# Performance work log

Measured on AMD Instinct MI355X. Metric: run time of the kernel, lower is better.

Reference implementation:

```python
import jax, jax.numpy as jnp
import numpy as np
from jax import lax

B, T, H, THETA_DIM = 64, 2048, 256, 5
L1, L2, OUT = 256, 256, 1


def _p(key, shape, fan_in):
    return jax.random.normal(key, shape, dtype=jnp.float32) / np.sqrt(fan_in)


def setup_inputs() -> dict:
    key = jax.random.key(0)
    ks = jax.random.split(key, 16)
    inp = {
        "x": jax.random.normal(ks[0], (B, T), dtype=jnp.float32),
        "theta": jax.random.normal(ks[1], (B, THETA_DIM), dtype=jnp.float32),
        # LSTM layer 0 (input dim 1): gate order [i, f, g, o]
        "Wx0": _p(ks[2], (1, 4 * H), 1),
        "Wh0": _p(ks[3], (H, 4 * H), H),
        "b0": jnp.zeros((4 * H,), dtype=jnp.float32),
        # LSTM layer 1 (input dim H)
        "Wx1": _p(ks[4], (H, 4 * H), H),
        "Wh1": _p(ks[5], (H, 4 * H), H),
        "b1": jnp.zeros((4 * H,), dtype=jnp.float32),
        # theta projector Dense(H)
        "Wtp": _p(ks[6], (THETA_DIM, H), THETA_DIM),
        "btp": jnp.zeros((H,), dtype=jnp.float32),
        # MLP head: concat(H + H) -> 256 -> 256 -> 1
        "Wl1": _p(ks[7], (2 * H, L1), 2 * H),
        "bl1": jnp.zeros((L1,), dtype=jnp.float32),
        "Wl2": _p(ks[8], (L1, L2), L1),
        "bl2": jnp.zeros((L2,), dtype=jnp.float32),
        "Wo": _p(ks[9], (L2, OUT), L2),
        "bo": jnp.zeros((OUT,), dtype=jnp.float32),
    }
    return inp


def _lstm_layer(x_seq, Wx, Wh, b):
    # x_seq: [B, T, D]. Precompute input-to-gate GEMM once (big, batched),
    # leaving only the small recurrent matmul inside the scan.
    xg = jnp.einsum('btd,dg->btg', x_seq, Wx) + b  # [B, T, 4H]
    bsz = x_seq.shape[0]
    h = Wh.shape[0]
    c0 = jnp.zeros((bsz, h), dtype=x_seq.dtype)
    h0 = jnp.zeros((bsz, h), dtype=x_seq.dtype)

    def step(carry, xg_t):
        c, hh = carry
        gates = xg_t + hh @ Wh  # [B, 4H]
        i, f, g, o = jnp.split(gates, 4, axis=-1)
        c = jax.nn.sigmoid(f) * c + jax.nn.sigmoid(i) * jnp.tanh(g)
        hh = jax.nn.sigmoid(o) * jnp.tanh(c)
        return (c, hh), hh

    _, hs = lax.scan(step, (c0, h0), jnp.swapaxes(xg, 0, 1))  # hs: [T, B, H]
    return jnp.swapaxes(hs, 0, 1)  # [B, T, H]


def reference(x, theta, Wx0, Wh0, b0, Wx1, Wh1, b1, Wtp, btp,
              Wl1, bl1, Wl2, bl2, Wo, bo):
    h = x[:, :, None]  # [B, T, 1] (module expands 2-D input)
    h = _lstm_layer(h, Wx0, Wh0, b0)
    h = _lstm_layer(h, Wx1, Wh1, b1)
    h = jnp.mean(h, axis=1)  # mean_aggregation=True -> [B, H]
    tproj = theta @ Wtp + btp  # [B, H]
    z = jnp.concatenate([h, tproj], axis=-1)  # [B, 2H]
    z = jax.nn.elu(z @ Wl1 + bl1)
    z = jax.nn.elu(z @ Wl2 + bl2)
    return z @ Wo + bo  # [B, 1]
```

## Files before the change

### kernel.cpp

```cpp
#include <hip/hip_runtime.h>
#include <hip/hip_bf16.h>


#define BB 64
#define TT 2048
#define HH 256
#define D0 16
#define D1 4

typedef short s16x8 __attribute__((ext_vector_type(8)));
typedef float f32x4 __attribute__((ext_vector_type(4)));

__device__ inline unsigned short f2bf(float f) {
  unsigned u = __float_as_uint(f);
  u += 0x7fff + ((u >> 16) & 1);
  return (unsigned short)(u >> 16);
}
__device__ inline float sigm(float x) { return 1.f / (1.f + __expf(-x)); }
__device__ inline float tanh_f(float x) { return 1.f - 2.f / (__expf(2.f * x) + 1.f); }

__device__ inline unsigned long long ld64(const unsigned int* p) {
  return __hip_atomic_load((const unsigned long long*)p, __ATOMIC_RELAXED,
                           __HIP_MEMORY_SCOPE_AGENT);
}
__device__ inline void st32(unsigned int* p, unsigned int v) {
  __hip_atomic_store(p, v, __ATOMIC_RELAXED, __HIP_MEMORY_SCOPE_AGENT);
}
__device__ inline void st32i(int* p, int v) {
  __hip_atomic_store(p, v, __ATOMIC_RELAXED, __HIP_MEMORY_SCOPE_AGENT);
}
__device__ inline int ld32i(const int* p) {
  return __hip_atomic_load(p, __ATOMIC_RELAXED, __HIP_MEMORY_SCOPE_AGENT);
}
__device__ inline void wg_bar() {
  asm volatile("s_waitcnt lgkmcnt(0)" ::: "memory");
  __builtin_amdgcn_sched_barrier(0);
  __builtin_amdgcn_s_barrier();
  __builtin_amdgcn_sched_barrier(0);
}
__device__ inline bool tag2ok(unsigned long long q, unsigned int tg) {
  return (((q >> 16) & 0xFFFFu) == tg) & ((unsigned)(q >> 48) == tg);
}

#define MFMA(a, b, c) __builtin_amdgcn_mfma_f32_16x16x32_bf16((a), (b), (c), 0, 0, 0)

__global__ void xt_kernel(const float* __restrict__ x, float* __restrict__ xT) {
  int i = blockIdx.x * 256 + threadIdx.x;
  int b = i & 63, t = i >> 6;
  xT[(size_t)t * BB + b] = x[(size_t)b * TT + t];
}

__global__ __launch_bounds__(512, 1)
void lstm_kernel(const float* __restrict__ Wx0, const float* __restrict__ Wh0,
                 const float* __restrict__ b0v,
                 const float* __restrict__ Wx1, const float* __restrict__ Wh1,
                 const float* __restrict__ b1v,
                 const float* __restrict__ xT,
                 unsigned int* __restrict__ seqring,
                 unsigned int* __restrict__ h1ring,
                 float* __restrict__ hmean, int* prog)
{
  __shared__ __align__(16) char Ab [8192];
  __shared__ __align__(16) char Ab1[8192];
  __shared__ float gbuf[16][4][66];

  const int tid  = threadIdx.x;
  const int lane = tid & 63;
  const int w    = tid >> 6;
  const int u16  = lane & 15;
  const int kgrp = lane >> 4;
  const int arow = lane & 15;
  const int bid  = blockIdx.x;

  if (bid < 8) {
    const int g = bid >> 1, ho = bid & 1, po = 1 - ho;
    const int U = ho * 128 + w * 16 + u16;
    s16x8 bw[32];
#pragma unroll
    for (int n = 0; n < 4; ++n)
#pragma unroll
      for (int ph = 0; ph < 2; ++ph)
#pragma unroll
        for (int i = 0; i < 4; ++i) {
          const int ks = (ph == 0 ? ho : po) * 4 + i;
          const int col = n * 256 + U;
#pragma unroll
          for (int j = 0; j < 8; ++j)
            bw[n * 8 + ph * 4 + i][j] =
                (short)f2bf(Wh0[(size_t)(ks * 32 + kgrp * 8 + j) * 1024 + col]);
        }
    float bE[4], xE[4];
#pragma unroll
    for (int n = 0; n < 4; ++n) { bE[n] = b0v[n * 256 + U]; xE[n] = Wx0[n * 256 + U]; }

    unsigned int* sr = seqring + (size_t)g * D0 * 4096;
    const int srow = tid >> 5, spc = (tid & 31) * 4;
    float cL[4] = {0.f, 0.f, 0.f, 0.f};
    unsigned long long pq0 = 0, pq1 = 0;

    for (int t = 0; t < TT; ++t) {
      if ((t & 7) == 0 && t >= 16 && tid < 4)
        while (ld32i(&prog[(g * 4 + tid) * 16]) < t - 8) __builtin_amdgcn_s_sleep(8);
      wg_bar();

      const unsigned int* sb = sr + ((t - 1) & (D0 - 1)) * 4096 + srow * 256 + po * 128 + spc;
      unsigned long long r0 = 0, r1 = 0;
      if (t > 0) { r0 = ld64(sb); r1 = ld64(sb + 2); }
      float xr[4];
#pragma unroll
      for (int r = 0; r < 4; ++r) xr[r] = xT[(size_t)t * BB + g * 16 + kgrp * 4 + r];

      f32x4 acc[4] = {{0,0,0,0},{0,0,0,0},{0,0,0,0},{0,0,0,0}};
      if (t > 0) {
        s16x8 ao[4];
#pragma unroll
        for (int i = 0; i < 4; ++i) {
          const int ks = ho * 4 + i;
          ao[i] = *(const s16x8*)(Ab + ((arow * 512 + (ks * 32 + kgrp * 8) * 2) ^ ((arow & 7) << 4)));
        }
#pragma unroll
        for (int i = 0; i < 4; ++i)
#pragma unroll
          for (int n = 0; n < 4; ++n) acc[n] = MFMA(ao[i], bw[n * 8 + i], acc[n]);
        const unsigned int tg = (unsigned int)t;
        unsigned long long q0 = pq0, q1 = pq1;
        for (;;) {
          if (__all(tag2ok(q0, tg) & tag2ok(q1, tg))) break;
          q0 = r0; q1 = r1;
          r0 = ld64(sb); r1 = ld64(sb + 2);
        }
        const unsigned int lo = (unsigned)(q0 & 0xFFFF) | (((unsigned)(q0 >> 32) & 0xFFFF) << 16);
        const unsigned int hi = (unsigned)(q1 & 0xFFFF) | (((unsigned)(q1 >> 32) & 0xFFFF) << 16);
        *(uint2*)(Ab + ((srow * 512 + (po * 128 + spc) * 2) ^ ((srow & 7) << 4))) = (uint2){lo, hi};
      }
      wg_bar();
      if (t > 0) {
        s16x8 ap[4];
#pragma unroll
        for (int i = 0; i < 4; ++i) {
          const int ks = po * 4 + i;
          ap[i] = *(const s16x8*)(Ab + ((arow * 512 + (ks * 32 + kgrp * 8) * 2) ^ ((arow & 7) << 4)));
        }
#pragma unroll
        for (int i = 0; i < 4; ++i)
#pragma unroll
          for (int n = 0; n < 4; ++n) acc[n] = MFMA(ap[i], bw[n * 8 + 4 + i], acc[n]);
      }
      const unsigned int tagw = (unsigned)(t + 1) << 16;
#pragma unroll
      for (int r = 0; r < 4; ++r) {
        const int row = kgrp * 4 + r;
        const float gi = acc[0][r] + bE[0] + xr[r] * xE[0];
        const float gf = acc[1][r] + bE[1] + xr[r] * xE[1];
        const float gg = acc[2][r] + bE[2] + xr[r] * xE[2];
        const float go = acc[3][r] + bE[3] + xr[r] * xE[3];
        cL[r] = sigm(gf) * cL[r] + sigm(gi) * tanh_f(gg);
        const float hv = sigm(go) * tanh_f(cL[r]);
        const unsigned short hb = f2bf(hv);
        st32(sr + (t & (D0 - 1)) * 4096 + row * 256 + U, tagw | hb);
        *(unsigned short*)(Ab + ((row * 512 + U * 2) ^ ((row & 7) << 4))) = hb;
      }
      {
        const unsigned int* pb = sr + (t & (D0 - 1)) * 4096 + srow * 256 + po * 128 + spc;
        pq0 = ld64(pb); pq1 = ld64(pb + 2);
      }
    }
  } else {
    const int idx = bid - 8, g = idx >> 2, q = idx & 3;
    const int gp = w >> 2;
    const int uo = (w & 3) * 16;
    const int ub = q * 64;
    s16x8 bw[2][16];
#pragma unroll
    for (int nt = 0; nt < 2; ++nt)
#pragma unroll
      for (int ks = 0; ks < 16; ++ks) {
        const int col = (2 * gp + nt) * 256 + ub + uo + u16;
#pragma unroll
        for (int j = 0; j < 8; ++j) {
          const int k = (ks & 7) * 32 + kgrp * 8 + j;
          bw[nt][ks][j] = (short)f2bf((ks < 8) ? Wx1[(size_t)k * 1024 + col]
                                               : Wh1[(size_t)k * 1024 + col]);
        }
      }
    const int eur = tid >> 5, eu2 = (tid & 31) * 2;
    float bE[4][2];
#pragma unroll
    for (int ga = 0; ga < 4; ++ga)
#pragma unroll
      for (int uu = 0; uu < 2; ++uu)
        bE[ga][uu] = b1v[ga * 256 + ub + eu2 + uu];

    unsigned int* sr = seqring + (size_t)g * D0 * 4096;
    unsigned int* hr = h1ring  + (size_t)g * D1 * 4096;
    const int srow = tid >> 5, sc8 = (tid & 31) * 8;
    float cL[2] = {0.f, 0.f}, hs[2] = {0.f, 0.f};
    unsigned long long qh0[4], qh1[4];

    {
      const unsigned int* sb = sr + srow * 256 + sc8;
#pragma unroll
      for (int i = 0; i < 4; ++i) qh0[i] = ld64(sb + i * 2);
    }

    for (int t = 0; t < TT; ++t) {
      if ((t & 3) == 3 && tid == 0) st32i(&prog[(g * 4 + q) * 16], t);
      const unsigned int* sbh1 = hr + ((t - 1) & (D1 - 1)) * 4096 + srow * 256 + sc8;
      unsigned long long rh1[4];
      if (t > 0) {
#pragma unroll
        for (int i = 0; i < 4; ++i) rh1[i] = ld64(sbh1 + i * 2);
      }
      {
        const unsigned int* sb = sr + (t & (D0 - 1)) * 4096 + srow * 256 + sc8;
        const unsigned int tg = (unsigned int)(t + 1);
        for (;;) {
          bool ok = true;
#pragma unroll
          for (int i = 0; i < 4; ++i) ok &= tag2ok(qh0[i], tg);
          if (__all(ok)) break;
#pragma unroll
          for (int i = 0; i < 4; ++i) qh0[i] = ld64(sb + i * 2);
        }
        unsigned int wv[4];
#pragma unroll
        for (int i = 0; i < 4; ++i)
          wv[i] = (unsigned)(qh0[i] & 0xFFFF) | (((unsigned)(qh0[i] >> 32) & 0xFFFF) << 16);
        *(uint4*)(Ab + ((srow * 512 + sc8 * 2) ^ ((srow & 7) << 4))) =
            (uint4){wv[0], wv[1], wv[2], wv[3]};
      }
      wg_bar();
      f32x4 acc0 = {0,0,0,0}, acc1 = {0,0,0,0};
      {
        s16x8 a[8];
#pragma unroll
        for (int ks = 0; ks < 8; ++ks)
          a[ks] = *(const s16x8*)(Ab + ((arow * 512 + (ks * 32 + kgrp * 8) * 2) ^ ((arow & 7) << 4)));
#pragma unroll
        for (int ks = 0; ks < 8; ++ks) {
          acc0 = MFMA(a[ks], bw[0][ks], acc0);
          acc1 = MFMA(a[ks], bw[1][ks], acc1);
        }
      }
      if (t > 0) {
        const unsigned int tg = (unsigned int)t;
        for (;;) {
          bool ok = true;
#pragma unroll
          for (int i = 0; i < 4; ++i) ok &= tag2ok(qh1[i], tg);
          if (__all(ok)) break;
#pragma unroll
          for (int i = 0; i < 4; ++i) qh1[i] = rh1[i];
#pragma unroll
          for (int i = 0; i < 4; ++i) rh1[i] = ld64(sbh1 + i * 2);
        }
        unsigned int wv[4];
#pragma unroll
        for (int i = 0; i < 4; ++i)
          wv[i] = (unsigned)(qh1[i] & 0xFFFF) | (((unsigned)(qh1[i] >> 32) & 0xFFFF) << 16);
        *(uint4*)(Ab1 + ((srow * 512 + sc8 * 2) ^ ((srow & 7) << 4))) =
            (uint4){wv[0], wv[1], wv[2], wv[3]};
      }
      wg_bar();
      if (t > 0) {
        s16x8 a[8];
#pragma unroll
        for (int kk = 0; kk < 8; ++kk)
          a[kk] = *(const s16x8*)(Ab1 + ((arow * 512 + (kk * 32 + kgrp * 8) * 2) ^ ((arow & 7) << 4)));
#pragma unroll
        for (int kk = 0; kk < 8; ++kk) {
          acc0 = MFMA(a[kk], bw[0][8 + kk], acc0);
          acc1 = MFMA(a[kk], bw[1][8 + kk], acc1);
        }
      }
#pragma unroll
      for (int r = 0; r < 4; ++r) {
        gbuf[kgrp * 4 + r][2 * gp + 0][uo + u16] = acc0[r];
        gbuf[kgrp * 4 + r][2 * gp + 1][uo + u16] = acc1[r];
      }
      wg_bar();

      unsigned short hb[2];
#pragma unroll
      for (int uu = 0; uu < 2; ++uu) {
        const int u = eu2 + uu;
        const float gi = gbuf[eur][0][u] + bE[0][uu];
        const float gf = gbuf[eur][1][u] + bE[1][uu];
        const float gg = gbuf[eur][2][u] + bE[2][uu];
        const float go = gbuf[eur][3][u] + bE[3][uu];
        cL[uu] = sigm(gf) * cL[uu] + sigm(gi) * tanh_f(gg);
        const float hv = sigm(go) * tanh_f(cL[uu]);
        hs[uu] += hv;
        hb[uu] = f2bf(hv);
      }
      const unsigned int tagw = (unsigned)(t + 1) << 16;
      st32(hr + (t & (D1 - 1)) * 4096 + eur * 256 + ub + eu2,     tagw | hb[0]);
      st32(hr + (t & (D1 - 1)) * 4096 + eur * 256 + ub + eu2 + 1, tagw | hb[1]);
      {
        const unsigned int* sb = sr + ((t + 1) & (D0 - 1)) * 4096 + srow * 256 + sc8;
#pragma unroll
        for (int i = 0; i < 4; ++i) qh0[i] = ld64(sb + i * 2);
        const unsigned int* hb2 = hr + (t & (D1 - 1)) * 4096 + srow * 256 + sc8;
#pragma unroll
        for (int i = 0; i < 4; ++i) qh1[i] = ld64(hb2 + i * 2);
      }
    }
#pragma unroll
    for (int uu = 0; uu < 2; ++uu)
      hmean[(size_t)(g * 16 + eur) * HH + ub + eu2 + uu] = hs[uu] * (1.f / TT);
  }
}

__global__ __launch_bounds__(256)
void mlp_kernel(const float* __restrict__ theta, const float* __restrict__ Wtp,
                const float* __restrict__ btp, const float* __restrict__ Wl1,
                const float* __restrict__ bl1, const float* __restrict__ Wl2,
                const float* __restrict__ bl2, const float* __restrict__ Wo,
                const float* __restrict__ bo, const float* __restrict__ hmean,
                float* __restrict__ out)
{
  const int b = blockIdx.x;
  const int j = threadIdx.x;
  __shared__ float z[2 * HH];
  __shared__ float z1s[HH];
  __shared__ float red[256];

  float tp = btp[j];
#pragma unroll
  for (int d = 0; d < 5; ++d) tp += theta[b * 5 + d] * Wtp[d * HH + j];
  z[j] = hmean[(size_t)b * HH + j];
  z[HH + j] = tp;
  __syncthreads();

  float a1 = bl1[j];
  for (int k = 0; k < 2 * HH; ++k) a1 += z[k] * Wl1[(size_t)k * 256 + j];
  a1 = (a1 > 0.f) ? a1 : (__expf(a1) - 1.f);
  z1s[j] = a1;
  __syncthreads();

  float a2 = bl2[j];
  for (int k = 0; k < HH; ++k) a2 += z1s[k] * Wl2[(size_t)k * 256 + j];
  a2 = (a2 > 0.f) ? a2 : (__expf(a2) - 1.f);
  red[j] = a2 * Wo[j];
  __syncthreads();
  for (int s = 128; s > 0; s >>= 1) {
    if (j < s) red[j] += red[j + s];
    __syncthreads();
  }
  if (j == 0) out[b] = red[0] + bo[0];
}

extern "C" void kernel_launch(void* const* d_in, const int* in_sizes, int n_in,
                              void* d_out, int out_size, void* d_ws, size_t ws_size,
                              hipStream_t stream) {
  const float* x    = (const float*)d_in[0];
  const float* theta= (const float*)d_in[1];
  const float* Wx0  = (const float*)d_in[2];
  const float* Wh0  = (const float*)d_in[3];
  const float* b0   = (const float*)d_in[4];
  const float* Wx1  = (const float*)d_in[5];
  const float* Wh1  = (const float*)d_in[6];
  const float* b1   = (const float*)d_in[7];
  const float* Wtp  = (const float*)d_in[8];
  const float* btp  = (const float*)d_in[9];
  const float* Wl1  = (const float*)d_in[10];
  const float* bl1  = (const float*)d_in[11];
  const float* Wl2  = (const float*)d_in[12];
  const float* bl2  = (const float*)d_in[13];
  const float* Wo   = (const float*)d_in[14];
  const float* bo   = (const float*)d_in[15];

  char* ws = (char*)d_ws;
  int* prog             = (int*)ws;
  unsigned int* seqring = (unsigned int*)(ws + 8192);
  unsigned int* h1ring  = (unsigned int*)(ws + 8192 + 1048576);
  float* hmean          = (float*)(ws + 8192 + 1048576 + 262144);
  float* xT             = (float*)(ws + 8192 + 1048576 + 262144 + 65536);
  const size_t WS_NEED = 8192ull + 1048576 + 262144 + 65536 + 524288;
  if (ws_size < WS_NEED) return;

  hipMemsetAsync(d_ws, 0, 8192 + 1048576 + 262144, stream);

  xt_kernel<<<dim3((BB * TT) / 256), dim3(256), 0, stream>>>(x, xT);
  lstm_kernel<<<dim3(24), dim3(512), 0, stream>>>(
      Wx0, Wh0, b0, Wx1, Wh1, b1, xT, seqring, h1ring, hmean, prog);
  mlp_kernel<<<dim3(BB), dim3(256), 0, stream>>>(
      theta, Wtp, btp, Wl1, bl1, Wl2, bl2, Wo, bo, hmean, (float*)d_out);
}
```

Baseline: 6.900 ms.

## Pin LSTM batch groups to one XCD and poll ring buffers through L2

The grid grows to 48 blocks, and blocks with bid&7 >= 4 exit at once, so each batch group's cooperating blocks land on the same XCD under round-robin dispatch. Inter-block h exchanges are then published with an sc0 store plus an agent-scope store, and polled with sc0 loads meant to hit the shared L2. After eight failed polls the loop falls back to agent-scope loads. The old software-prefetched double-buffered polling is replaced by s_sleep backoff, which trades prefetch overlap for cheaper, XCD-local spin latency and relies on an undocumented block-to-XCD mapping.

```diff
diff --git a/kernel.cpp b/kernel.cpp
--- a/kernel.cpp
+++ b/kernel.cpp
@@ -19,11 +19,11 @@
 __device__ inline float sigm(float x) { return 1.f / (1.f + __expf(-x)); }
 __device__ inline float tanh_f(float x) { return 1.f - 2.f / (__expf(2.f * x) + 1.f); }
 
-__device__ inline unsigned long long ld64(const unsigned int* p) {
+__device__ inline unsigned long long ld64_ag(const unsigned int* p) {
   return __hip_atomic_load((const unsigned long long*)p, __ATOMIC_RELAXED,
                            __HIP_MEMORY_SCOPE_AGENT);
 }
-__device__ inline void st32(unsigned int* p, unsigned int v) {
+__device__ inline void st32_ag(unsigned int* p, unsigned int v) {
   __hip_atomic_store(p, v, __ATOMIC_RELAXED, __HIP_MEMORY_SCOPE_AGENT);
 }
 __device__ inline void st32i(int* p, int v) {
@@ -31,6 +31,17 @@
 }
 __device__ inline int ld32i(const int* p) {
   return __hip_atomic_load(p, __ATOMIC_RELAXED, __HIP_MEMORY_SCOPE_AGENT);
+}
+__device__ inline unsigned long long ld64_l2(const unsigned int* p) {
+  unsigned long long v;
+  asm volatile("global_load_dwordx2 %0, %1, off sc0\n\ts_waitcnt vmcnt(0)"
+               : "=&v"(v) : "v"(p) : "memory");
+  __builtin_amdgcn_sched_barrier(0);
+  return v;
+}
+__device__ inline void st32_pub(unsigned int* p, unsigned int v) {
+  asm volatile("global_store_dword %0, %1, off sc0" :: "v"(p), "v"(v) : "memory");
+  __hip_atomic_store(p, v, __ATOMIC_RELAXED, __HIP_MEMORY_SCOPE_AGENT);
 }
 __device__ inline void wg_bar() {
   asm volatile("s_waitcnt lgkmcnt(0)" ::: "memory");
@@ -64,16 +75,20 @@
   __shared__ __align__(16) char Ab1[8192];
   __shared__ float gbuf[16][4][66];
 
+  const int bid = blockIdx.x;
+  const int g   = bid & 7;
+  const int rid = bid >> 3;
+  if (g >= 4) return;
+
   const int tid  = threadIdx.x;
   const int lane = tid & 63;
   const int w    = tid >> 6;
   const int u16  = lane & 15;
   const int kgrp = lane >> 4;
   const int arow = lane & 15;
-  const int bid  = blockIdx.x;
-
-  if (bid < 8) {
-    const int g = bid >> 1, ho = bid & 1, po = 1 - ho;
+
+  if (rid < 2) {
+    const int ho = rid, po = 1 - ho;
     const int U = ho * 128 + w * 16 + u16;
     s16x8 bw[32];
 #pragma unroll
@@ -104,8 +119,6 @@
       wg_bar();
 
       const unsigned int* sb = sr + ((t - 1) & (D0 - 1)) * 4096 + srow * 256 + po * 128 + spc;
-      unsigned long long r0 = 0, r1 = 0;
-      if (t > 0) { r0 = ld64(sb); r1 = ld64(sb + 2); }
       float xr[4];
 #pragma unroll
       for (int r = 0; r < 4; ++r) xr[r] = xT[(size_t)t * BB + g * 16 + kgrp * 4 + r];
@@ -124,10 +137,13 @@
           for (int n = 0; n < 4; ++n) acc[n] = MFMA(ao[i], bw[n * 8 + i], acc[n]);
         const unsigned int tg = (unsigned int)t;
         unsigned long long q0 = pq0, q1 = pq1;
+        int att = 0;
         for (;;) {
           if (__all(tag2ok(q0, tg) & tag2ok(q1, tg))) break;
-          q0 = r0; q1 = r1;
-          r0 = ld64(sb); r1 = ld64(sb + 2);
+          __builtin_amdgcn_s_sleep(1);
+          if (att < 8) { q0 = ld64_l2(sb); q1 = ld64_l2(sb + 2); }
+          else         { q0 = ld64_ag(sb); q1 = ld64_ag(sb + 2); }
+          ++att;
         }
         const unsigned int lo = (unsigned)(q0 & 0xFFFF) | (((unsigned)(q0 >> 32) & 0xFFFF) << 16);
         const unsigned int hi = (unsigned)(q1 & 0xFFFF) | (((unsigned)(q1 >> 32) & 0xFFFF) << 16);
@@ -157,16 +173,16 @@
         cL[r] = sigm(gf) * cL[r] + sigm(gi) * tanh_f(gg);
         const float hv = sigm(go) * tanh_f(cL[r]);
         const unsigned short hb = f2bf(hv);
-        st32(sr + (t & (D0 - 1)) * 4096 + row * 256 + U, tagw | hb);
+        st32_pub(sr + (t & (D0 - 1)) * 4096 + row * 256 + U, tagw | hb);
         *(unsigned short*)(Ab + ((row * 512 + U * 2) ^ ((row & 7) << 4))) = hb;
       }
       {
         const unsigned int* pb = sr + (t & (D0 - 1)) * 4096 + srow * 256 + po * 128 + spc;
-        pq0 = ld64(pb); pq1 = ld64(pb + 2);
+        pq0 = ld64_l2(pb); pq1 = ld64_l2(pb + 2);
       }
     }
   } else {
-    const int idx = bid - 8, g = idx >> 2, q = idx & 3;
+    const int q = rid - 2;
     const int gp = w >> 2;
     const int uo = (w & 3) * 16;
     const int ub = q * 64;
@@ -200,27 +216,29 @@
     {
       const unsigned int* sb = sr + srow * 256 + sc8;
 #pragma unroll
-      for (int i = 0; i < 4; ++i) qh0[i] = ld64(sb + i * 2);
+      for (int i = 0; i < 4; ++i) qh0[i] = ld64_l2(sb + i * 2);
     }
 
     for (int t = 0; t < TT; ++t) {
       if ((t & 3) == 3 && tid == 0) st32i(&prog[(g * 4 + q) * 16], t);
-      const unsigned int* sbh1 = hr + ((t - 1) & (D1 - 1)) * 4096 + srow * 256 + sc8;
-      unsigned long long rh1[4];
-      if (t > 0) {
-#pragma unroll
-        for (int i = 0; i < 4; ++i) rh1[i] = ld64(sbh1 + i * 2);
-      }
       {
         const unsigned int* sb = sr + (t & (D0 - 1)) * 4096 + srow * 256 + sc8;
         const unsigned int tg = (unsigned int)(t + 1);
+        int att = 0;
         for (;;) {
           bool ok = true;
 #pragma unroll
           for (int i = 0; i < 4; ++i) ok &= tag2ok(qh0[i], tg);
           if (__all(ok)) break;
-#pragma unroll
-          for (int i = 0; i < 4; ++i) qh0[i] = ld64(sb + i * 2);
+          __builtin_amdgcn_s_sleep(1);
+          if (att < 8) {
+#pragma unroll
+            for (int i = 0; i < 4; ++i) qh0[i] = ld64_l2(sb + i * 2);
+          } else {
+#pragma unroll
+            for (int i = 0; i < 4; ++i) qh0[i] = ld64_ag(sb + i * 2);
+          }
+          ++att;
         }
         unsigned int wv[4];
 #pragma unroll
@@ -243,16 +261,23 @@
         }
       }
       if (t > 0) {
+        const unsigned int* sbh1 = hr + ((t - 1) & (D1 - 1)) * 4096 + srow * 256 + sc8;
         const unsigned int tg = (unsigned int)t;
+        int att = 0;
         for (;;) {
           bool ok = true;
 #pragma unroll
           for (int i = 0; i < 4; ++i) ok &= tag2ok(qh1[i], tg);
           if (__all(ok)) break;
-#pragma unroll
-          for (int i = 0; i < 4; ++i) qh1[i] = rh1[i];
-#pragma unroll
-          for (int i = 0; i < 4; ++i) rh1[i] = ld64(sbh1 + i * 2);
+          __builtin_amdgcn_s_sleep(1);
+          if (att < 8) {
+#pragma unroll
+            for (int i = 0; i < 4; ++i) qh1[i] = ld64_l2(sbh1 + i * 2);
+          } else {
+#pragma unroll
+            for (int i = 0; i < 4; ++i) qh1[i] = ld64_ag(sbh1 + i * 2);
+          }
+          ++att;
         }
         unsigned int wv[4];
 #pragma unroll
@@ -294,15 +319,15 @@
         hb[uu] = f2bf(hv);
       }
       const unsigned int tagw = (unsigned)(t + 1) << 16;
-      st32(hr + (t & (D1 - 1)) * 4096 + eur * 256 + ub + eu2,     tagw | hb[0]);
-      st32(hr + (t & (D1 - 1)) * 4096 + eur * 256 + ub + eu2 + 1, tagw | hb[1]);
+      st32_pub(hr + (t & (D1 - 1)) * 4096 + eur * 256 + ub + eu2,     tagw | hb[0]);
+      st32_pub(hr + (t & (D1 - 1)) * 4096 + eur * 256 + ub + eu2 + 1, tagw | hb[1]);
       {
         const unsigned int* sb = sr + ((t + 1) & (D0 - 1)) * 4096 + srow * 256 + sc8;
 #pragma unroll
-        for (int i = 0; i < 4; ++i) qh0[i] = ld64(sb + i * 2);
+        for (int i = 0; i < 4; ++i) qh0[i] = ld64_l2(sb + i * 2);
         const unsigned int* hb2 = hr + (t & (D1 - 1)) * 4096 + srow * 256 + sc8;
 #pragma unroll
-        for (int i = 0; i < 4; ++i) qh1[i] = ld64(hb2 + i * 2);
+        for (int i = 0; i < 4; ++i) qh1[i] = ld64_l2(hb2 + i * 2);
       }
     }
 #pragma unroll
@@ -382,7 +407,7 @@
   hipMemsetAsync(d_ws, 0, 8192 + 1048576 + 262144, stream);
 
   xt_kernel<<<dim3((BB * TT) / 256), dim3(256), 0, stream>>>(x, xT);
-  lstm_kernel<<<dim3(24), dim3(512), 0, stream>>>(
+  lstm_kernel<<<dim3(48), dim3(512), 0, stream>>>(
       Wx0, Wh0, b0, Wx1, Wh1, b1, xT, seqring, h1ring, hmean, prog);
   mlp_kernel<<<dim3(BB), dim3(256), 0, stream>>>(
       theta, Wtp, btp, Wl1, bl1, Wl2, bl2, Wo, bo, hmean, (float*)d_out);
```

Result: slower. 13.26 ms (+92.2%).

## Decouple LSTM layer 1 from layer 0 via full-sequence buffer and flags

Applied to the files above, without the earlier changes.

Layer 0 now writes its packed bf16 hidden state for every timestep to a full-length sequence buffer and publishes a per-block progress flag after a drain barrier. Layer 1 polls these flags and prefetches the next step's input, instead of tag-polling a small ring, and the backpressure from layer 1 to layer 0 is removed. The separate x-transpose kernel is dropped in favour of strided reads of x, and the ring depths are reduced. In exchange it adds a workspace buffer of several tens of MB and a full memory drain every layer-0 step, which may lengthen that recurrent critical path.

```diff
diff --git a/kernel.cpp b/kernel.cpp
--- a/kernel.cpp
+++ b/kernel.cpp
@@ -5,8 +5,8 @@
 #define BB 64
 #define TT 2048
 #define HH 256
-#define D0 16
-#define D1 4
+#define D0 4
+#define D1 2
 
 typedef short s16x8 __attribute__((ext_vector_type(8)));
 typedef float f32x4 __attribute__((ext_vector_type(4)));
@@ -38,39 +38,43 @@
   __builtin_amdgcn_s_barrier();
   __builtin_amdgcn_sched_barrier(0);
 }
+__device__ inline void drain_bar() {
+  asm volatile("s_waitcnt vmcnt(0) lgkmcnt(0)" ::: "memory");
+  __builtin_amdgcn_sched_barrier(0);
+  __builtin_amdgcn_s_barrier();
+  __builtin_amdgcn_sched_barrier(0);
+}
 __device__ inline bool tag2ok(unsigned long long q, unsigned int tg) {
   return (((q >> 16) & 0xFFFFu) == tg) & ((unsigned)(q >> 48) == tg);
 }
 
 #define MFMA(a, b, c) __builtin_amdgcn_mfma_f32_16x16x32_bf16((a), (b), (c), 0, 0, 0)
-
-__global__ void xt_kernel(const float* __restrict__ x, float* __restrict__ xT) {
-  int i = blockIdx.x * 256 + threadIdx.x;
-  int b = i & 63, t = i >> 6;
-  xT[(size_t)t * BB + b] = x[(size_t)b * TT + t];
-}
 
 __global__ __launch_bounds__(512, 1)
 void lstm_kernel(const float* __restrict__ Wx0, const float* __restrict__ Wh0,
                  const float* __restrict__ b0v,
                  const float* __restrict__ Wx1, const float* __restrict__ Wh1,
                  const float* __restrict__ b1v,
-                 const float* __restrict__ xT,
+                 const float* __restrict__ x,
                  unsigned int* __restrict__ seqring,
                  unsigned int* __restrict__ h1ring,
-                 float* __restrict__ hmean, int* prog)
+                 unsigned int* __restrict__ seq0p,
+                 float* __restrict__ hmean, int* flags)
 {
   __shared__ __align__(16) char Ab [8192];
   __shared__ __align__(16) char Ab1[8192];
   __shared__ float gbuf[16][4][66];
-
+  __shared__ int smem_seen;
+
+  const int bid  = blockIdx.x;
   const int tid  = threadIdx.x;
   const int lane = tid & 63;
   const int w    = tid >> 6;
   const int u16  = lane & 15;
   const int kgrp = lane >> 4;
   const int arow = lane & 15;
-  const int bid  = blockIdx.x;
+
+  int* f0 = flags + 512;
 
   if (bid < 8) {
     const int g = bid >> 1, ho = bid & 1, po = 1 - ho;
@@ -94,22 +98,17 @@
     for (int n = 0; n < 4; ++n) { bE[n] = b0v[n * 256 + U]; xE[n] = Wx0[n * 256 + U]; }
 
     unsigned int* sr = seqring + (size_t)g * D0 * 4096;
+    int* myflag = &f0[(g * 2 + ho) * 16];
     const int srow = tid >> 5, spc = (tid & 31) * 4;
     float cL[4] = {0.f, 0.f, 0.f, 0.f};
     unsigned long long pq0 = 0, pq1 = 0;
 
     for (int t = 0; t < TT; ++t) {
-      if ((t & 7) == 0 && t >= 16 && tid < 4)
-        while (ld32i(&prog[(g * 4 + tid) * 16]) < t - 8) __builtin_amdgcn_s_sleep(8);
-      wg_bar();
+      float xr[4];
+#pragma unroll
+      for (int r = 0; r < 4; ++r) xr[r] = x[(size_t)(g * 16 + kgrp * 4 + r) * TT + t];
 
       const unsigned int* sb = sr + ((t - 1) & (D0 - 1)) * 4096 + srow * 256 + po * 128 + spc;
-      unsigned long long r0 = 0, r1 = 0;
-      if (t > 0) { r0 = ld64(sb); r1 = ld64(sb + 2); }
-      float xr[4];
-#pragma unroll
-      for (int r = 0; r < 4; ++r) xr[r] = xT[(size_t)t * BB + g * 16 + kgrp * 4 + r];
-
       f32x4 acc[4] = {{0,0,0,0},{0,0,0,0},{0,0,0,0},{0,0,0,0}};
       if (t > 0) {
         s16x8 ao[4];
@@ -126,8 +125,8 @@
         unsigned long long q0 = pq0, q1 = pq1;
         for (;;) {
           if (__all(tag2ok(q0, tg) & tag2ok(q1, tg))) break;
-          q0 = r0; q1 = r1;
-          r0 = ld64(sb); r1 = ld64(sb + 2);
+          __builtin_amdgcn_s_sleep(1);
+          q0 = ld64(sb); q1 = ld64(sb + 2);
         }
         const unsigned int lo = (unsigned)(q0 & 0xFFFF) | (((unsigned)(q0 >> 32) & 0xFFFF) << 16);
         const unsigned int hi = (unsigned)(q1 & 0xFFFF) | (((unsigned)(q1 >> 32) & 0xFFFF) << 16);
@@ -159,7 +158,14 @@
         const unsigned short hb = f2bf(hv);
         st32(sr + (t & (D0 - 1)) * 4096 + row * 256 + U, tagw | hb);
         *(unsigned short*)(Ab + ((row * 512 + U * 2) ^ ((row & 7) << 4))) = hb;
-      }
+        const float ov = __shfl_xor(hv, 1);
+        if ((u16 & 1) == 0) {
+          const unsigned int pk = (unsigned)hb | ((unsigned)f2bf(ov) << 16);
+          st32(seq0p + ((size_t)t * BB + g * 16 + row) * 128 + (U >> 1), pk);
+        }
+      }
+      drain_bar();
+      if (tid == 0) st32i(myflag, t + 1);
       {
         const unsigned int* pb = sr + (t & (D0 - 1)) * 4096 + srow * 256 + po * 128 + spc;
         pq0 = ld64(pb); pq1 = ld64(pb + 2);
@@ -191,43 +197,44 @@
       for (int uu = 0; uu < 2; ++uu)
         bE[ga][uu] = b1v[ga * 256 + ub + eu2 + uu];
 
-    unsigned int* sr = seqring + (size_t)g * D0 * 4096;
-    unsigned int* hr = h1ring  + (size_t)g * D1 * 4096;
-    const int srow = tid >> 5, sc8 = (tid & 31) * 8;
+    unsigned int* hr = h1ring + (size_t)g * D1 * 4096;
+    int* fA = &f0[(g * 2 + 0) * 16];
+    int* fB = &f0[(g * 2 + 1) * 16];
+    const int srow = tid >> 5;
+    const int sc8  = (tid & 31) * 8;
+    const int k4   = (tid & 31) * 4;
     float cL[2] = {0.f, 0.f}, hs[2] = {0.f, 0.f};
-    unsigned long long qh0[4], qh1[4];
-
-    {
-      const unsigned int* sb = sr + srow * 256 + sc8;
-#pragma unroll
-      for (int i = 0; i < 4; ++i) qh0[i] = ld64(sb + i * 2);
-    }
+    unsigned long long qh1[4];
+    uint4 pf_h0;
+    bool pf = false;
+
+    if (tid == 0) smem_seen = 0;
+    __syncthreads();
 
     for (int t = 0; t < TT; ++t) {
-      if ((t & 3) == 3 && tid == 0) st32i(&prog[(g * 4 + q) * 16], t);
-      const unsigned int* sbh1 = hr + ((t - 1) & (D1 - 1)) * 4096 + srow * 256 + sc8;
-      unsigned long long rh1[4];
-      if (t > 0) {
-#pragma unroll
-        for (int i = 0; i < 4; ++i) rh1[i] = ld64(sbh1 + i * 2);
-      }
-      {
-        const unsigned int* sb = sr + (t & (D0 - 1)) * 4096 + srow * 256 + sc8;
-        const unsigned int tg = (unsigned int)(t + 1);
-        for (;;) {
-          bool ok = true;
-#pragma unroll
-          for (int i = 0; i < 4; ++i) ok &= tag2ok(qh0[i], tg);
-          if (__all(ok)) break;
-#pragma unroll
-          for (int i = 0; i < 4; ++i) qh0[i] = ld64(sb + i * 2);
-        }
-        unsigned int wv[4];
-#pragma unroll
-        for (int i = 0; i < 4; ++i)
-          wv[i] = (unsigned)(qh0[i] & 0xFFFF) | (((unsigned)(qh0[i] >> 32) & 0xFFFF) << 16);
-        *(uint4*)(Ab + ((srow * 512 + sc8 * 2) ^ ((srow & 7) << 4))) =
-            (uint4){wv[0], wv[1], wv[2], wv[3]};
+      uint4 h0v;
+      if (pf) {
+        h0v = pf_h0;
+      } else {
+        if (tid == 0) {
+          int s = smem_seen;
+          if (s < t + 1) {
+            do { int a = ld32i(fA), b = ld32i(fB); s = a < b ? a : b;
+                 if (s < t + 1) __builtin_amdgcn_s_sleep(2); } while (s < t + 1);
+          }
+          smem_seen = s;
+        }
+        wg_bar();
+        h0v = *(const uint4*)(seq0p + ((size_t)t * BB + g * 16 + srow) * 128 + k4);
+      }
+      *(uint4*)(Ab + ((srow * 512 + k4 * 4) ^ ((srow & 7) << 4))) = h0v;
+      if (tid == 0) {
+        int s0 = smem_seen;
+        if (s0 < t + 3) {
+          int a = ld32i(fA), b = ld32i(fB);
+          int s = a < b ? a : b;
+          if (s > s0) smem_seen = s;
+        }
       }
       wg_bar();
       f32x4 acc0 = {0,0,0,0}, acc1 = {0,0,0,0};
@@ -243,16 +250,16 @@
         }
       }
       if (t > 0) {
+        const unsigned int* sbh1 = hr + ((t - 1) & (D1 - 1)) * 4096 + srow * 256 + sc8;
         const unsigned int tg = (unsigned int)t;
         for (;;) {
           bool ok = true;
 #pragma unroll
           for (int i = 0; i < 4; ++i) ok &= tag2ok(qh1[i], tg);
           if (__all(ok)) break;
-#pragma unroll
-          for (int i = 0; i < 4; ++i) qh1[i] = rh1[i];
-#pragma unroll
-          for (int i = 0; i < 4; ++i) rh1[i] = ld64(sbh1 + i * 2);
+          __builtin_amdgcn_s_sleep(1);
+#pragma unroll
+          for (int i = 0; i < 4; ++i) qh1[i] = ld64(sbh1 + i * 2);
         }
         unsigned int wv[4];
 #pragma unroll
@@ -296,10 +303,11 @@
       const unsigned int tagw = (unsigned)(t + 1) << 16;
       st32(hr + (t & (D1 - 1)) * 4096 + eur * 256 + ub + eu2,     tagw | hb[0]);
       st32(hr + (t & (D1 - 1)) * 4096 + eur * 256 + ub + eu2 + 1, tagw | hb[1]);
+      const int sE = smem_seen;
+      pf = (sE >= t + 2) && (t + 1 < TT);
+      if (pf)
+        pf_h0 = *(const uint4*)(seq0p + ((size_t)(t + 1) * BB + g * 16 + srow) * 128 + k4);
       {
-        const unsigned int* sb = sr + ((t + 1) & (D0 - 1)) * 4096 + srow * 256 + sc8;
-#pragma unroll
-        for (int i = 0; i < 4; ++i) qh0[i] = ld64(sb + i * 2);
         const unsigned int* hb2 = hr + (t & (D1 - 1)) * 4096 + srow * 256 + sc8;
 #pragma unroll
         for (int i = 0; i < 4; ++i) qh1[i] = ld64(hb2 + i * 2);
@@ -371,19 +379,19 @@
   const float* bo   = (const float*)d_in[15];
 
   char* ws = (char*)d_ws;
-  int* prog             = (int*)ws;
+  int* flags            = (int*)ws;
   unsigned int* seqring = (unsigned int*)(ws + 8192);
-  unsigned int* h1ring  = (unsigned int*)(ws + 8192 + 1048576);
-  float* hmean          = (float*)(ws + 8192 + 1048576 + 262144);
-  float* xT             = (float*)(ws + 8192 + 1048576 + 262144 + 65536);
-  const size_t WS_NEED = 8192ull + 1048576 + 262144 + 65536 + 524288;
+  unsigned int* h1ring  = (unsigned int*)(ws + 8192 + 262144);
+  float* hmean          = (float*)(ws + 8192 + 262144 + 131072);
+  unsigned int* seq0p   = (unsigned int*)(ws + 8192 + 262144 + 131072 + 65536);
+  const size_t WS_NEED = 8192ull + 262144 + 131072 + 65536 +
+                         (size_t)TT * BB * 128 * 4ull;
   if (ws_size < WS_NEED) return;
 
-  hipMemsetAsync(d_ws, 0, 8192 + 1048576 + 262144, stream);
-
-  xt_kernel<<<dim3((BB * TT) / 256), dim3(256), 0, stream>>>(x, xT);
+  hipMemsetAsync(d_ws, 0, 8192 + 262144 + 131072, stream);
+
   lstm_kernel<<<dim3(24), dim3(512), 0, stream>>>(
-      Wx0, Wh0, b0, Wx1, Wh1, b1, xT, seqring, h1ring, hmean, prog);
+      Wx0, Wh0, b0, Wx1, Wh1, b1, x, seqring, h1ring, seq0p, hmean, flags);
   mlp_kernel<<<dim3(BB), dim3(256), 0, stream>>>(
       theta, Wtp, btp, Wl1, bl1, Wl2, bl2, Wo, bo, hmean, (float*)d_out);
 }
```

New measurement: 6.278 ms. 9.0% less time.
